# Kernel optimization log

Measured on AMD Instinct MI355X. Metric: run time of the kernel, lower is better.

Reference implementation:

```python
import jax, jax.numpy as jnp
import numpy as np

N_NODES = 100000
N_EDGES = 1250000
N_FEAT = 128
NHID = 64
NUM_GRAPHS = 256


def setup_inputs() -> dict:
    key = jax.random.key(0)
    ks = jax.random.split(key, 12)
    sc = lambda fan_in: 1.414 * (6.0 / fan_in) ** 0.5  # rough xavier-ish scale
    inp = {
        "x": jax.random.normal(ks[0], (N_NODES, N_FEAT), dtype=jnp.float32),
        "edge_attr": jax.random.uniform(ks[1], (N_EDGES, 5), dtype=jnp.float32),
        "W_e1": jax.random.normal(ks[2], (5, NHID), dtype=jnp.float32) * sc(5),
        "b_e1": jnp.zeros((NHID,), jnp.float32),
        "W_e2": jax.random.normal(ks[3], (NHID, NHID), dtype=jnp.float32) * sc(NHID),
        "b_e2": jnp.zeros((NHID,), jnp.float32),
        "W_e3": jax.random.normal(ks[4], (NHID, 1), dtype=jnp.float32) * sc(NHID),
        "b_e3": jnp.zeros((1,), jnp.float32),
        "W_g": jax.random.normal(ks[5], (N_FEAT, NHID), dtype=jnp.float32) * sc(N_FEAT),
        "b_g": jnp.zeros((NHID,), jnp.float32),
        "W_b1": jax.random.normal(ks[6], (NHID, NHID), dtype=jnp.float32) * sc(NHID),
        "b_b1": jnp.zeros((NHID,), jnp.float32),
        "W_b2": jax.random.normal(ks[7], (NHID, 1), dtype=jnp.float32) * sc(NHID),
        "b_b2": jnp.zeros((1,), jnp.float32),
        "edge_index": jax.random.randint(ks[8], (2, N_EDGES), 0, N_NODES, dtype=jnp.int64 if jax.config.jax_enable_x64 else jnp.int32),
        "batch": jnp.sort(jax.random.randint(ks[9], (N_NODES,), 0, NUM_GRAPHS, dtype=jnp.int64 if jax.config.jax_enable_x64 else jnp.int32)),
    }
    return inp


def _forward(x, edge_attr, W_e1, b_e1, W_e2, b_e2, W_e3, b_e3, W_g, b_g,
             W_b1, b_b1, W_b2, b_b2, edge_index, batch):
    N = x.shape[0]
    # edge MLP -> scalar weight per edge, then final ReLU (F.relu in forward)
    h = jax.nn.relu(edge_attr @ W_e1 + b_e1)
    h = jax.nn.relu(h @ W_e2 + b_e2)
    edge_w = jax.nn.relu((h @ W_e3 + b_e3)[:, 0])  # [E]

    row, col = edge_index[0], edge_index[1]
    # add self-loops with weight 1 (PyG GCNConv default)
    loop = jnp.arange(N, dtype=row.dtype)
    row_f = jnp.concatenate([row, loop])
    col_f = jnp.concatenate([col, loop])
    w_f = jnp.concatenate([edge_w, jnp.ones((N,), edge_w.dtype)])

    # symmetric normalization D^{-1/2} A_hat D^{-1/2}
    deg = jax.ops.segment_sum(w_f, col_f, num_segments=N)
    dinv = jnp.where(deg > 0, jax.lax.rsqrt(jnp.where(deg > 0, deg, 1.0)), 0.0)
    norm = dinv[row_f] * w_f * dinv[col_f]  # [E+N]

    xw = x @ W_g  # [N, nhid]
    agg = jax.ops.segment_sum(xw[row_f] * norm[:, None], col_f, num_segments=N)
    node = jax.nn.relu(agg + b_g)  # dropout is identity in eval mode

    pooled = jax.ops.segment_sum(node, batch, num_segments=NUM_GRAPHS)  # [G, nhid]
    z = jax.nn.relu(pooled @ W_b1 + b_b1)
    logits = z @ W_b2 + b_b2  # [G, 1]
    return logits


def reference(x, edge_attr, W_e1, b_e1, W_e2, b_e2, W_e3, b_e3, W_g, b_g,
              W_b1, b_b1, W_b2, b_b2, edge_index, batch):
    return _forward(x, edge_attr, W_e1, b_e1, W_e2, b_e2, W_e3, b_e3, W_g, b_g,
                    W_b1, b_b1, W_b2, b_b2, edge_index, batch)
```

## Files before the change

### kernel.cpp

```cpp
#include <hip/hip_runtime.h>
#include <hip/hip_bf16.h>

#define N_NODES 100000
#define N_EDGES 1250000
#define N_FEAT 128
#define NHID 64
#define NUM_GRAPHS 256
#define NB_SCAN 98

typedef __attribute__((ext_vector_type(8))) short short8;
typedef __attribute__((ext_vector_type(16))) float float16;
typedef __attribute__((ext_vector_type(4))) int int4v;

static __device__ __forceinline__ short f2bf(float x) {
    __hip_bfloat16 b = __float2bfloat16(x);
    return *reinterpret_cast<short*>(&b);
}
static __device__ __forceinline__ float bf2f(short s) {
    __hip_bfloat16 b = *reinterpret_cast<__hip_bfloat16*>(&s);
    return __bfloat162float(b);
}
static __device__ __forceinline__ int pk2(float a, float b) {
    unsigned lo = (unsigned short)f2bf(a);
    unsigned hi = (unsigned short)f2bf(b);
    return (int)(lo | (hi << 16));
}

__global__ void k0_init(int* __restrict__ cnt, float* __restrict__ pooled) {
    int i = blockIdx.x * blockDim.x + threadIdx.x;
    if (i < N_NODES) cnt[i] = 0;
    if (i < NUM_GRAPHS * NHID) pooled[i] = 0.0f;
}

__global__ __launch_bounds__(256) void k1_edge_mlp(
    const float* __restrict__ ea, const float* __restrict__ W1,
    const float* __restrict__ b1, const float* __restrict__ W2,
    const float* __restrict__ b2, const float* __restrict__ W3,
    const float* __restrict__ b3, const int* __restrict__ eidx,
    float* __restrict__ edge_w, int* __restrict__ cnt)
{
    const int lane = threadIdx.x & 63;
    const int l31 = lane & 31;
    const int h = lane >> 5;
    const int wslot = blockIdx.x * 4 + (threadIdx.x >> 6);
    const int S = gridDim.x * 4;
    const float b3v = b3[0];

    short8 a1hi[2], a1lo[2];
    #pragma unroll
    for (int t = 0; t < 2; ++t)
        #pragma unroll
        for (int j = 0; j < 8; ++j) {
            int k = 8 * h + j;
            float v = (k < 5) ? W1[k * NHID + t * 32 + l31] : 0.0f;
            short hi = f2bf(v);
            a1hi[t][j] = hi;
            a1lo[t][j] = f2bf(v - bf2f(hi));
        }

    float b1r[2][16];
    #pragma unroll
    for (int t = 0; t < 2; ++t)
        #pragma unroll
        for (int r = 0; r < 16; ++r)
            b1r[t][r] = b1[t * 32 + (r & 3) + 8 * (r >> 2) + 4 * h];

    short8 afrag[2][4];
    #pragma unroll
    for (int t = 0; t < 2; ++t)
        #pragma unroll
        for (int kk = 0; kk < 4; ++kk)
            #pragma unroll
            for (int j = 0; j < 8; ++j) {
                int k = kk * 16 + h * 8 + j;
                afrag[t][kk][j] = f2bf(W2[k * NHID + t * 32 + l31]);
            }

    float b2r[2][16], w3r[2][16];
    #pragma unroll
    for (int t = 0; t < 2; ++t)
        #pragma unroll
        for (int r = 0; r < 16; ++r) {
            int hid = t * 32 + (r & 3) + 8 * (r >> 2) + 4 * h;
            b2r[t][r] = b2[hid];
            w3r[t][r] = W3[hid];
        }

    const int NCHUNK = (N_EDGES + 31) / 32;

    float pe[5] = {0.f, 0.f, 0.f, 0.f, 0.f};
    if (wslot < NCHUNK && h == 0) {
        int e = wslot * 32 + l31;
        int ec = (e < N_EDGES) ? e : (N_EDGES - 1);
        #pragma unroll
        for (int j = 0; j < 5; ++j) pe[j] = ea[ec * 5 + j];
    }

    for (int chunk = wslot; chunk < NCHUNK; chunk += S) {
        int nchunk = chunk + S;
        float ne[5] = {0.f, 0.f, 0.f, 0.f, 0.f};
        if (nchunk < NCHUNK && h == 0) {
            int e2 = nchunk * 32 + l31;
            int ec2 = (e2 < N_EDGES) ? e2 : (N_EDGES - 1);
            #pragma unroll
            for (int j = 0; j < 5; ++j) ne[j] = ea[ec2 * 5 + j];
        }

        int e = chunk * 32 + l31;
        bool valid = e < N_EDGES;

        short8 behi, belo;
        #pragma unroll
        for (int j = 0; j < 8; ++j) {
            float v = (h == 0 && j < 5) ? pe[j] : 0.0f;
            short hi = f2bf(v);
            behi[j] = hi;
            belo[j] = f2bf(v - bf2f(hi));
        }

        float16 acc1a, acc1b;
        #pragma unroll
        for (int r = 0; r < 16; ++r) { acc1a[r] = b1r[0][r]; acc1b[r] = b1r[1][r]; }
        acc1a = __builtin_amdgcn_mfma_f32_32x32x16_bf16(a1hi[0], behi, acc1a, 0, 0, 0);
        acc1a = __builtin_amdgcn_mfma_f32_32x32x16_bf16(a1hi[0], belo, acc1a, 0, 0, 0);
        acc1a = __builtin_amdgcn_mfma_f32_32x32x16_bf16(a1lo[0], behi, acc1a, 0, 0, 0);
        acc1b = __builtin_amdgcn_mfma_f32_32x32x16_bf16(a1hi[1], behi, acc1b, 0, 0, 0);
        acc1b = __builtin_amdgcn_mfma_f32_32x32x16_bf16(a1hi[1], belo, acc1b, 0, 0, 0);
        acc1b = __builtin_amdgcn_mfma_f32_32x32x16_bf16(a1lo[1], behi, acc1b, 0, 0, 0);

        short8 bf2v[4];
        #pragma unroll
        for (int kk = 0; kk < 4; ++kk) {
            float lv0, lv1, lv2, lv3, hv0, hv1, hv2, hv3;
            if (kk >> 1) {
                int o = 8 * (kk & 1);
                lv0 = fmaxf(acc1b[o + 0], 0.f); lv1 = fmaxf(acc1b[o + 1], 0.f);
                lv2 = fmaxf(acc1b[o + 2], 0.f); lv3 = fmaxf(acc1b[o + 3], 0.f);
                hv0 = fmaxf(acc1b[o + 4], 0.f); hv1 = fmaxf(acc1b[o + 5], 0.f);
                hv2 = fmaxf(acc1b[o + 6], 0.f); hv3 = fmaxf(acc1b[o + 7], 0.f);
            } else {
                int o = 8 * (kk & 1);
                lv0 = fmaxf(acc1a[o + 0], 0.f); lv1 = fmaxf(acc1a[o + 1], 0.f);
                lv2 = fmaxf(acc1a[o + 2], 0.f); lv3 = fmaxf(acc1a[o + 3], 0.f);
                hv0 = fmaxf(acc1a[o + 4], 0.f); hv1 = fmaxf(acc1a[o + 5], 0.f);
                hv2 = fmaxf(acc1a[o + 6], 0.f); hv3 = fmaxf(acc1a[o + 7], 0.f);
            }
            int p_lv0 = pk2(lv0, lv1), p_lv1 = pk2(lv2, lv3);
            int p_hv0 = pk2(hv0, hv1), p_hv1 = pk2(hv2, hv3);
            int send0 = h ? p_lv0 : p_hv0;
            int send1 = h ? p_lv1 : p_hv1;
            int r0 = __shfl_xor(send0, 32, 64);
            int r1 = __shfl_xor(send1, 32, 64);
            int4v fi;
            fi.x = h ? r0 : p_lv0;
            fi.y = h ? r1 : p_lv1;
            fi.z = h ? p_hv0 : r0;
            fi.w = h ? p_hv1 : r1;
            bf2v[kk] = __builtin_bit_cast(short8, fi);
        }

        float16 c0, c1;
        #pragma unroll
        for (int r = 0; r < 16; ++r) { c0[r] = b2r[0][r]; c1[r] = b2r[1][r]; }
        #pragma unroll
        for (int kk = 0; kk < 4; ++kk) {
            c0 = __builtin_amdgcn_mfma_f32_32x32x16_bf16(afrag[0][kk], bf2v[kk], c0, 0, 0, 0);
            c1 = __builtin_amdgcn_mfma_f32_32x32x16_bf16(afrag[1][kk], bf2v[kk], c1, 0, 0, 0);
        }

        float partial = 0.0f;
        #pragma unroll
        for (int r = 0; r < 16; ++r) {
            partial += fmaxf(c0[r], 0.0f) * w3r[0][r];
            partial += fmaxf(c1[r], 0.0f) * w3r[1][r];
        }
        float total = partial + __shfl_xor(partial, 32, 64);
        float w = fmaxf(total + b3v, 0.0f);

        if (h == 0 && valid) {
            edge_w[e] = w;
            if (w > 0.0f) atomicAdd(&cnt[eidx[N_EDGES + e]], 1);
        }

        #pragma unroll
        for (int j = 0; j < 5; ++j) pe[j] = ne[j];
    }
}

__global__ __launch_bounds__(1024) void s1_blocksum(const int* __restrict__ cnt,
                                                    int* __restrict__ bsum) {
    __shared__ int sd[1024];
    int t = threadIdx.x;
    int i = blockIdx.x * 1024 + t;
    sd[t] = (i < N_NODES) ? cnt[i] : 0;
    __syncthreads();
    #pragma unroll
    for (int d = 512; d > 0; d >>= 1) {
        if (t < d) sd[t] += sd[t + d];
        __syncthreads();
    }
    if (t == 0) bsum[blockIdx.x] = sd[0];
}

__global__ __launch_bounds__(128) void s2_scanbase(const int* __restrict__ bsum,
                                                   int* __restrict__ bbase,
                                                   int* __restrict__ off) {
    __shared__ int sd[128];
    int t = threadIdx.x;
    int v = (t < NB_SCAN) ? bsum[t] : 0;
    sd[t] = v;
    __syncthreads();
    #pragma unroll
    for (int d = 1; d < 128; d <<= 1) {
        int u = (t >= d) ? sd[t - d] : 0;
        __syncthreads();
        sd[t] += u;
        __syncthreads();
    }
    if (t < NB_SCAN) bbase[t] = sd[t] - v;
    if (t == 127) off[N_NODES] = sd[127];
}

__global__ __launch_bounds__(1024) void s3_blockscan(const int* __restrict__ cnt,
                                                     const int* __restrict__ bbase,
                                                     int* __restrict__ off,
                                                     int* __restrict__ cur) {
    __shared__ int sd[1024];
    int t = threadIdx.x;
    int i = blockIdx.x * 1024 + t;
    int c = (i < N_NODES) ? cnt[i] : 0;
    sd[t] = c;
    __syncthreads();
    #pragma unroll
    for (int d = 1; d < 1024; d <<= 1) {
        int v = (t >= d) ? sd[t - d] : 0;
        __syncthreads();
        sd[t] += v;
        __syncthreads();
    }
    if (i < N_NODES) {
        int ex = sd[t] - c + bbase[blockIdx.x];
        off[i] = ex;
        cur[i] = ex;
    }
}

__global__ void k_place(const float* __restrict__ edge_w, const int* __restrict__ eidx,
                        int* __restrict__ cur, int2* __restrict__ recs) {
    int e = blockIdx.x * 256 + threadIdx.x;
    if (e >= N_EDGES) return;
    float w = edge_w[e];
    if (w <= 0.0f) return;
    int col = eidx[N_EDGES + e];
    int pos = atomicAdd(&cur[col], 1);
    recs[pos] = make_int2(eidx[e], __float_as_int(w));
}

__global__ void k_deg(const int* __restrict__ off, const int2* __restrict__ recs,
                      float* __restrict__ dinv) {
    int n = blockIdx.x * 256 + threadIdx.x;
    if (n >= N_NODES) return;
    int o0 = off[n], o1 = off[n + 1];
    float s = 1.0f;
    for (int j = o0; j < o1; ++j) s += __int_as_float(recs[j].y);
    dinv[n] = rsqrtf(s);
}

__global__ __launch_bounds__(256) void k3_xw(
    const float* __restrict__ x, const float* __restrict__ Wg,
    const float* __restrict__ dinv, float* __restrict__ xws)
{
    const int lane = threadIdx.x & 63;
    const int l31 = lane & 31;
    const int h = lane >> 5;
    const int wslot = blockIdx.x * 4 + (threadIdx.x >> 6);

    short8 bw[8][2];
    #pragma unroll
    for (int kk = 0; kk < 8; ++kk)
        #pragma unroll
        for (int u = 0; u < 2; ++u)
            #pragma unroll
            for (int j = 0; j < 8; ++j)
                bw[kk][u][j] = f2bf(Wg[(kk * 16 + 8 * h + j) * NHID + u * 32 + l31]);

    const int NC = N_NODES / 32;
    for (int chunk = wslot; chunk < NC; chunk += gridDim.x * 4) {
        int base = chunk * 32;
        const float* xrow = x + (size_t)(base + l31) * N_FEAT + 8 * h;

        float16 acc0, acc1;
        #pragma unroll
        for (int r = 0; r < 16; ++r) { acc0[r] = 0.0f; acc1[r] = 0.0f; }

        #pragma unroll
        for (int kk = 0; kk < 8; ++kk) {
            float4 p = *(const float4*)(xrow + kk * 16);
            float4 q = *(const float4*)(xrow + kk * 16 + 4);
            short8 af;
            af[0] = f2bf(p.x); af[1] = f2bf(p.y); af[2] = f2bf(p.z); af[3] = f2bf(p.w);
            af[4] = f2bf(q.x); af[5] = f2bf(q.y); af[6] = f2bf(q.z); af[7] = f2bf(q.w);
            acc0 = __builtin_amdgcn_mfma_f32_32x32x16_bf16(af, bw[kk][0], acc0, 0, 0, 0);
            acc1 = __builtin_amdgcn_mfma_f32_32x32x16_bf16(af, bw[kk][1], acc1, 0, 0, 0);
        }

        #pragma unroll
        for (int r = 0; r < 16; ++r) {
            int node = base + (r & 3) + 8 * (r >> 2) + 4 * h;
            float dv = dinv[node];
            xws[node * NHID + l31] = acc0[r] * dv;
            xws[node * NHID + 32 + l31] = acc1[r] * dv;
        }
    }
}

__global__ __launch_bounds__(256) void k4_gather_pool(
    const int* __restrict__ off, const int2* __restrict__ recs,
    const float* __restrict__ xws, const float* __restrict__ dinv,
    const float* __restrict__ bg, const int* __restrict__ batch,
    float* __restrict__ pooled)
{
    const int lane = threadIdx.x & 63;
    const int wv = blockIdx.x * 4 + (threadIdx.x >> 6);
    int n0 = wv * 8;
    if (n0 >= N_NODES) return;
    float bgl = bg[lane];
    float pacc = 0.0f;
    int curg = batch[n0];
    #pragma unroll
    for (int nn = 0; nn < 8; ++nn) {
        int n = n0 + nn;
        int g = batch[n];
        if (g != curg) {
            atomicAdd(&pooled[curg * NHID + lane], pacc);
            pacc = 0.0f;
            curg = g;
        }
        int o0 = off[n], o1 = off[n + 1];
        float acc = xws[(size_t)n * NHID + lane];
        if (o0 < o1) {
            int2 r = recs[o0];
            float gth = xws[(size_t)r.x * NHID + lane];
            for (int j = o0; j < o1 - 1; ++j) {
                int2 rn = recs[j + 1];
                float gn = xws[(size_t)rn.x * NHID + lane];
                acc = fmaf(__int_as_float(r.y), gth, acc);
                r = rn; gth = gn;
            }
            acc = fmaf(__int_as_float(r.y), gth, acc);
        }
        pacc += fmaxf(dinv[n] * acc + bgl, 0.0f);
    }
    atomicAdd(&pooled[curg * NHID + lane], pacc);
}

__global__ __launch_bounds__(64) void k6_final(
    const float* __restrict__ pooled, const float* __restrict__ Wb1,
    const float* __restrict__ bb1, const float* __restrict__ Wb2,
    const float* __restrict__ bb2, float* __restrict__ out) {
    __shared__ float p[NHID];
    int lane = threadIdx.x;
    int g = blockIdx.x;
    p[lane] = pooled[g * NHID + lane];
    __syncthreads();
    float z = bb1[lane];
    #pragma unroll
    for (int k = 0; k < NHID; ++k) z += p[k] * Wb1[k * NHID + lane];
    z = fmaxf(z, 0.0f) * Wb2[lane];
    #pragma unroll
    for (int off = 32; off > 0; off >>= 1)
        z += __shfl_down(z, off, 64);
    if (lane == 0) out[g] = z + bb2[0];
}

extern "C" void kernel_launch(void* const* d_in, const int* in_sizes, int n_in,
                              void* d_out, int out_size, void* d_ws, size_t ws_size,
                              hipStream_t stream) {
    const float* x        = (const float*)d_in[0];
    const float* ea       = (const float*)d_in[1];
    const float* W_e1     = (const float*)d_in[2];
    const float* b_e1     = (const float*)d_in[3];
    const float* W_e2     = (const float*)d_in[4];
    const float* b_e2     = (const float*)d_in[5];
    const float* W_e3     = (const float*)d_in[6];
    const float* b_e3     = (const float*)d_in[7];
    const float* W_g      = (const float*)d_in[8];
    const float* b_g      = (const float*)d_in[9];
    const float* W_b1     = (const float*)d_in[10];
    const float* b_b1     = (const float*)d_in[11];
    const float* W_b2     = (const float*)d_in[12];
    const float* b_b2     = (const float*)d_in[13];
    const int*   eidx     = (const int*)d_in[14];
    const int*   batch    = (const int*)d_in[15];
    float* out = (float*)d_out;

    char* wsb = (char*)d_ws;
    float* edge_w = (float*)wsb;
    int*   cnt    = (int*)(wsb + 4 * 1250048);
    int*   off    = (int*)(wsb + 4 * 1350080);
    int*   cur    = (int*)(wsb + 4 * 1450112);
    int*   bsum   = (int*)(wsb + 4 * 1550144);
    int*   bbase  = (int*)(wsb + 4 * 1550272);
    float* dinv   = (float*)(wsb + 4 * 1550400);
    float* pooled = (float*)(wsb + 4 * 1650432);
    int2*  recs   = (int2*)(wsb + 4 * 1666880);
    float* xws    = (float*)(wsb + 4 * 4166880);

    k0_init<<<dim3(391), dim3(256), 0, stream>>>(cnt, pooled);
    k1_edge_mlp<<<dim3(2048), dim3(256), 0, stream>>>(
        ea, W_e1, b_e1, W_e2, b_e2, W_e3, b_e3, eidx, edge_w, cnt);
    s1_blocksum<<<dim3(NB_SCAN), dim3(1024), 0, stream>>>(cnt, bsum);
    s2_scanbase<<<dim3(1), dim3(128), 0, stream>>>(bsum, bbase, off);
    s3_blockscan<<<dim3(NB_SCAN), dim3(1024), 0, stream>>>(cnt, bbase, off, cur);
    k_place<<<dim3((N_EDGES + 255) / 256), dim3(256), 0, stream>>>(edge_w, eidx, cur, recs);
    k_deg<<<dim3((N_NODES + 255) / 256), dim3(256), 0, stream>>>(off, recs, dinv);
    k3_xw<<<dim3(512), dim3(256), 0, stream>>>(x, W_g, dinv, xws);
    k4_gather_pool<<<dim3(3125), dim3(256), 0, stream>>>(off, recs, xws, dinv, b_g, batch, pooled);
    k6_final<<<dim3(NUM_GRAPHS), dim3(64), 0, stream>>>(pooled, W_b1, b_b1, W_b2, b_b2, out);
}
```

Before: 233.3 us.

## Fuse degree computation into edge MLP, fold biases into MFMA, retune gather

The edge MLP now processes two 32-edge chunks per iteration and folds the b1 and b2 biases into the MFMA operands through a constant-one column. It also atomically accumulates float degrees, which removes the separate k_deg pass; dinv is computed inside the block scan. The init kernel is replaced by a memset. The gather kernel handles 4 nodes per wave with a 4-way unrolled edge loop, and the grid sizes change. The cost is extra float atomics per edge, and the bf16 rounding of the b2 bias is a small accuracy risk.

```diff
diff --git a/kernel.cpp b/kernel.cpp
--- a/kernel.cpp
+++ b/kernel.cpp
@@ -26,18 +26,12 @@
     return (int)(lo | (hi << 16));
 }
 
-__global__ void k0_init(int* __restrict__ cnt, float* __restrict__ pooled) {
-    int i = blockIdx.x * blockDim.x + threadIdx.x;
-    if (i < N_NODES) cnt[i] = 0;
-    if (i < NUM_GRAPHS * NHID) pooled[i] = 0.0f;
-}
-
 __global__ __launch_bounds__(256) void k1_edge_mlp(
     const float* __restrict__ ea, const float* __restrict__ W1,
     const float* __restrict__ b1, const float* __restrict__ W2,
     const float* __restrict__ b2, const float* __restrict__ W3,
     const float* __restrict__ b3, const int* __restrict__ eidx,
-    float* __restrict__ edge_w, int* __restrict__ cnt)
+    float* __restrict__ edge_w, int* __restrict__ cnt, float* __restrict__ degf)
 {
     const int lane = threadIdx.x & 63;
     const int l31 = lane & 31;
@@ -52,19 +46,13 @@
         #pragma unroll
         for (int j = 0; j < 8; ++j) {
             int k = 8 * h + j;
-            float v = (k < 5) ? W1[k * NHID + t * 32 + l31] : 0.0f;
+            int m = t * 32 + l31;
+            float v = (k < 5) ? W1[k * NHID + m] : ((k == 5) ? b1[m] : 0.0f);
             short hi = f2bf(v);
             a1hi[t][j] = hi;
             a1lo[t][j] = f2bf(v - bf2f(hi));
         }
 
-    float b1r[2][16];
-    #pragma unroll
-    for (int t = 0; t < 2; ++t)
-        #pragma unroll
-        for (int r = 0; r < 16; ++r)
-            b1r[t][r] = b1[t * 32 + (r & 3) + 8 * (r >> 2) + 4 * h];
-
     short8 afrag[2][4];
     #pragma unroll
     for (int t = 0; t < 2; ++t)
@@ -76,114 +64,139 @@
                 afrag[t][kk][j] = f2bf(W2[k * NHID + t * 32 + l31]);
             }
 
-    float b2r[2][16], w3r[2][16];
+    short8 a2b[2], bone;
     #pragma unroll
     for (int t = 0; t < 2; ++t)
         #pragma unroll
-        for (int r = 0; r < 16; ++r) {
-            int hid = t * 32 + (r & 3) + 8 * (r >> 2) + 4 * h;
-            b2r[t][r] = b2[hid];
-            w3r[t][r] = W3[hid];
-        }
+        for (int j = 0; j < 8; ++j)
+            a2b[t][j] = (h == 0 && j == 0) ? f2bf(b2[t * 32 + l31]) : (short)0;
+    #pragma unroll
+    for (int j = 0; j < 8; ++j)
+        bone[j] = (h == 0 && j == 0) ? f2bf(1.0f) : (short)0;
+
+    float w3r[2][16];
+    #pragma unroll
+    for (int t = 0; t < 2; ++t)
+        #pragma unroll
+        for (int r = 0; r < 16; ++r)
+            w3r[t][r] = W3[t * 32 + (r & 3) + 8 * (r >> 2) + 4 * h];
 
     const int NCHUNK = (N_EDGES + 31) / 32;
-
-    float pe[5] = {0.f, 0.f, 0.f, 0.f, 0.f};
-    if (wslot < NCHUNK && h == 0) {
-        int e = wslot * 32 + l31;
-        int ec = (e < N_EDGES) ? e : (N_EDGES - 1);
-        #pragma unroll
-        for (int j = 0; j < 5; ++j) pe[j] = ea[ec * 5 + j];
-    }
-
-    for (int chunk = wslot; chunk < NCHUNK; chunk += S) {
-        int nchunk = chunk + S;
-        float ne[5] = {0.f, 0.f, 0.f, 0.f, 0.f};
-        if (nchunk < NCHUNK && h == 0) {
-            int e2 = nchunk * 32 + l31;
-            int ec2 = (e2 < N_EDGES) ? e2 : (N_EDGES - 1);
-            #pragma unroll
-            for (int j = 0; j < 5; ++j) ne[j] = ea[ec2 * 5 + j];
-        }
-
-        int e = chunk * 32 + l31;
-        bool valid = e < N_EDGES;
-
-        short8 behi, belo;
-        #pragma unroll
-        for (int j = 0; j < 8; ++j) {
-            float v = (h == 0 && j < 5) ? pe[j] : 0.0f;
-            short hi = f2bf(v);
-            behi[j] = hi;
-            belo[j] = f2bf(v - bf2f(hi));
-        }
-
-        float16 acc1a, acc1b;
-        #pragma unroll
-        for (int r = 0; r < 16; ++r) { acc1a[r] = b1r[0][r]; acc1b[r] = b1r[1][r]; }
-        acc1a = __builtin_amdgcn_mfma_f32_32x32x16_bf16(a1hi[0], behi, acc1a, 0, 0, 0);
-        acc1a = __builtin_amdgcn_mfma_f32_32x32x16_bf16(a1hi[0], belo, acc1a, 0, 0, 0);
-        acc1a = __builtin_amdgcn_mfma_f32_32x32x16_bf16(a1lo[0], behi, acc1a, 0, 0, 0);
-        acc1b = __builtin_amdgcn_mfma_f32_32x32x16_bf16(a1hi[1], behi, acc1b, 0, 0, 0);
-        acc1b = __builtin_amdgcn_mfma_f32_32x32x16_bf16(a1hi[1], belo, acc1b, 0, 0, 0);
-        acc1b = __builtin_amdgcn_mfma_f32_32x32x16_bf16(a1lo[1], behi, acc1b, 0, 0, 0);
-
-        short8 bf2v[4];
-        #pragma unroll
-        for (int kk = 0; kk < 4; ++kk) {
-            float lv0, lv1, lv2, lv3, hv0, hv1, hv2, hv3;
-            if (kk >> 1) {
+    const int PAIRS = (NCHUNK + 1) / 2;
+
+    for (int p = wslot; p < PAIRS; p += S) {
+        int ch[2] = {2 * p, 2 * p + 1};
+
+        short8 behi[2], belo[2];
+        bool cvq[2];
+        #pragma unroll
+        for (int q = 0; q < 2; ++q) {
+            int e = ch[q] * 32 + l31;
+            cvq[q] = (ch[q] < NCHUNK) && (e < N_EDGES);
+            int ec = (e < N_EDGES) ? e : (N_EDGES - 1);
+            #pragma unroll
+            for (int j = 0; j < 8; ++j) {
+                float v = 0.0f;
+                if (h == 0) {
+                    if (j < 5) v = ea[ec * 5 + j];
+                    else if (j == 5) v = 1.0f;
+                }
+                short hi = f2bf(v);
+                behi[q][j] = hi;
+                belo[q][j] = (h == 0 && j < 5) ? f2bf(v - bf2f(hi)) : (short)0;
+            }
+        }
+
+        float16 A1[2][2];
+        #pragma unroll
+        for (int q = 0; q < 2; ++q)
+            #pragma unroll
+            for (int t = 0; t < 2; ++t)
+                #pragma unroll
+                for (int r = 0; r < 16; ++r) A1[q][t][r] = 0.0f;
+        #pragma unroll
+        for (int t = 0; t < 2; ++t)
+            #pragma unroll
+            for (int q = 0; q < 2; ++q) {
+                A1[q][t] = __builtin_amdgcn_mfma_f32_32x32x16_bf16(a1hi[t], behi[q], A1[q][t], 0, 0, 0);
+                A1[q][t] = __builtin_amdgcn_mfma_f32_32x32x16_bf16(a1hi[t], belo[q], A1[q][t], 0, 0, 0);
+                A1[q][t] = __builtin_amdgcn_mfma_f32_32x32x16_bf16(a1lo[t], behi[q], A1[q][t], 0, 0, 0);
+            }
+
+        short8 bf2v[2][4];
+        #pragma unroll
+        for (int q = 0; q < 2; ++q) {
+            #pragma unroll
+            for (int kk = 0; kk < 4; ++kk) {
+                float lv0, lv1, lv2, lv3, hv0, hv1, hv2, hv3;
                 int o = 8 * (kk & 1);
-                lv0 = fmaxf(acc1b[o + 0], 0.f); lv1 = fmaxf(acc1b[o + 1], 0.f);
-                lv2 = fmaxf(acc1b[o + 2], 0.f); lv3 = fmaxf(acc1b[o + 3], 0.f);
-                hv0 = fmaxf(acc1b[o + 4], 0.f); hv1 = fmaxf(acc1b[o + 5], 0.f);
-                hv2 = fmaxf(acc1b[o + 6], 0.f); hv3 = fmaxf(acc1b[o + 7], 0.f);
-            } else {
-                int o = 8 * (kk & 1);
-                lv0 = fmaxf(acc1a[o + 0], 0.f); lv1 = fmaxf(acc1a[o + 1], 0.f);
-                lv2 = fmaxf(acc1a[o + 2], 0.f); lv3 = fmaxf(acc1a[o + 3], 0.f);
-                hv0 = fmaxf(acc1a[o + 4], 0.f); hv1 = fmaxf(acc1a[o + 5], 0.f);
-                hv2 = fmaxf(acc1a[o + 6], 0.f); hv3 = fmaxf(acc1a[o + 7], 0.f);
-            }
-            int p_lv0 = pk2(lv0, lv1), p_lv1 = pk2(lv2, lv3);
-            int p_hv0 = pk2(hv0, hv1), p_hv1 = pk2(hv2, hv3);
-            int send0 = h ? p_lv0 : p_hv0;
-            int send1 = h ? p_lv1 : p_hv1;
-            int r0 = __shfl_xor(send0, 32, 64);
-            int r1 = __shfl_xor(send1, 32, 64);
-            int4v fi;
-            fi.x = h ? r0 : p_lv0;
-            fi.y = h ? r1 : p_lv1;
-            fi.z = h ? p_hv0 : r0;
-            fi.w = h ? p_hv1 : r1;
-            bf2v[kk] = __builtin_bit_cast(short8, fi);
-        }
-
-        float16 c0, c1;
-        #pragma unroll
-        for (int r = 0; r < 16; ++r) { c0[r] = b2r[0][r]; c1[r] = b2r[1][r]; }
-        #pragma unroll
-        for (int kk = 0; kk < 4; ++kk) {
-            c0 = __builtin_amdgcn_mfma_f32_32x32x16_bf16(afrag[0][kk], bf2v[kk], c0, 0, 0, 0);
-            c1 = __builtin_amdgcn_mfma_f32_32x32x16_bf16(afrag[1][kk], bf2v[kk], c1, 0, 0, 0);
-        }
-
-        float partial = 0.0f;
-        #pragma unroll
-        for (int r = 0; r < 16; ++r) {
-            partial += fmaxf(c0[r], 0.0f) * w3r[0][r];
-            partial += fmaxf(c1[r], 0.0f) * w3r[1][r];
-        }
-        float total = partial + __shfl_xor(partial, 32, 64);
-        float w = fmaxf(total + b3v, 0.0f);
-
-        if (h == 0 && valid) {
-            edge_w[e] = w;
-            if (w > 0.0f) atomicAdd(&cnt[eidx[N_EDGES + e]], 1);
-        }
-
-        #pragma unroll
-        for (int j = 0; j < 5; ++j) pe[j] = ne[j];
+                if (kk >> 1) {
+                    lv0 = fmaxf(A1[q][1][o + 0], 0.f); lv1 = fmaxf(A1[q][1][o + 1], 0.f);
+                    lv2 = fmaxf(A1[q][1][o + 2], 0.f); lv3 = fmaxf(A1[q][1][o + 3], 0.f);
+                    hv0 = fmaxf(A1[q][1][o + 4], 0.f); hv1 = fmaxf(A1[q][1][o + 5], 0.f);
+                    hv2 = fmaxf(A1[q][1][o + 6], 0.f); hv3 = fmaxf(A1[q][1][o + 7], 0.f);
+                } else {
+                    lv0 = fmaxf(A1[q][0][o + 0], 0.f); lv1 = fmaxf(A1[q][0][o + 1], 0.f);
+                    lv2 = fmaxf(A1[q][0][o + 2], 0.f); lv3 = fmaxf(A1[q][0][o + 3], 0.f);
+                    hv0 = fmaxf(A1[q][0][o + 4], 0.f); hv1 = fmaxf(A1[q][0][o + 5], 0.f);
+                    hv2 = fmaxf(A1[q][0][o + 6], 0.f); hv3 = fmaxf(A1[q][0][o + 7], 0.f);
+                }
+                int p_lv0 = pk2(lv0, lv1), p_lv1 = pk2(lv2, lv3);
+                int p_hv0 = pk2(hv0, hv1), p_hv1 = pk2(hv2, hv3);
+                int send0 = h ? p_lv0 : p_hv0;
+                int send1 = h ? p_lv1 : p_hv1;
+                int r0 = __shfl_xor(send0, 32, 64);
+                int r1 = __shfl_xor(send1, 32, 64);
+                int4v fi;
+                fi.x = h ? r0 : p_lv0;
+                fi.y = h ? r1 : p_lv1;
+                fi.z = h ? p_hv0 : r0;
+                fi.w = h ? p_hv1 : r1;
+                bf2v[q][kk] = __builtin_bit_cast(short8, fi);
+            }
+        }
+
+        float16 C[2][2];
+        #pragma unroll
+        for (int q = 0; q < 2; ++q)
+            #pragma unroll
+            for (int t = 0; t < 2; ++t)
+                #pragma unroll
+                for (int r = 0; r < 16; ++r) C[q][t][r] = 0.0f;
+        #pragma unroll
+        for (int kk = 0; kk < 4; ++kk)
+            #pragma unroll
+            for (int q = 0; q < 2; ++q) {
+                C[q][0] = __builtin_amdgcn_mfma_f32_32x32x16_bf16(afrag[0][kk], bf2v[q][kk], C[q][0], 0, 0, 0);
+                C[q][1] = __builtin_amdgcn_mfma_f32_32x32x16_bf16(afrag[1][kk], bf2v[q][kk], C[q][1], 0, 0, 0);
+            }
+        #pragma unroll
+        for (int q = 0; q < 2; ++q) {
+            C[q][0] = __builtin_amdgcn_mfma_f32_32x32x16_bf16(a2b[0], bone, C[q][0], 0, 0, 0);
+            C[q][1] = __builtin_amdgcn_mfma_f32_32x32x16_bf16(a2b[1], bone, C[q][1], 0, 0, 0);
+        }
+
+        #pragma unroll
+        for (int q = 0; q < 2; ++q) {
+            float partial = 0.0f;
+            #pragma unroll
+            for (int r = 0; r < 16; ++r) {
+                partial += fmaxf(C[q][0][r], 0.0f) * w3r[0][r];
+                partial += fmaxf(C[q][1][r], 0.0f) * w3r[1][r];
+            }
+            float total = partial + __shfl_xor(partial, 32, 64);
+            float w = fmaxf(total + b3v, 0.0f);
+
+            if (h == 0 && cvq[q]) {
+                int e = ch[q] * 32 + l31;
+                edge_w[e] = w;
+                if (w > 0.0f) {
+                    int col = eidx[N_EDGES + e];
+                    atomicAdd(&cnt[col], 1);
+                    atomicAdd(&degf[col], w);
+                }
+            }
+        }
     }
 }
 
@@ -224,7 +237,9 @@
 __global__ __launch_bounds__(1024) void s3_blockscan(const int* __restrict__ cnt,
                                                      const int* __restrict__ bbase,
                                                      int* __restrict__ off,
-                                                     int* __restrict__ cur) {
+                                                     int* __restrict__ cur,
+                                                     const float* __restrict__ degf,
+                                                     float* __restrict__ dinv) {
     __shared__ int sd[1024];
     int t = threadIdx.x;
     int i = blockIdx.x * 1024 + t;
@@ -242,6 +257,7 @@
         int ex = sd[t] - c + bbase[blockIdx.x];
         off[i] = ex;
         cur[i] = ex;
+        dinv[i] = rsqrtf(1.0f + degf[i]);
     }
 }
 
@@ -256,16 +272,6 @@
     recs[pos] = make_int2(eidx[e], __float_as_int(w));
 }
 
-__global__ void k_deg(const int* __restrict__ off, const int2* __restrict__ recs,
-                      float* __restrict__ dinv) {
-    int n = blockIdx.x * 256 + threadIdx.x;
-    if (n >= N_NODES) return;
-    int o0 = off[n], o1 = off[n + 1];
-    float s = 1.0f;
-    for (int j = o0; j < o1; ++j) s += __int_as_float(recs[j].y);
-    dinv[n] = rsqrtf(s);
-}
-
 __global__ __launch_bounds__(256) void k3_xw(
     const float* __restrict__ x, const float* __restrict__ Wg,
     const float* __restrict__ dinv, float* __restrict__ xws)
@@ -322,14 +328,13 @@
 {
     const int lane = threadIdx.x & 63;
     const int wv = blockIdx.x * 4 + (threadIdx.x >> 6);
-    int n0 = wv * 8;
+    int n0 = wv * 4;
     if (n0 >= N_NODES) return;
+    int n1 = min(n0 + 4, N_NODES);
     float bgl = bg[lane];
     float pacc = 0.0f;
     int curg = batch[n0];
-    #pragma unroll
-    for (int nn = 0; nn < 8; ++nn) {
-        int n = n0 + nn;
+    for (int n = n0; n < n1; ++n) {
         int g = batch[n];
         if (g != curg) {
             atomicAdd(&pooled[curg * NHID + lane], pacc);
@@ -338,16 +343,21 @@
         }
         int o0 = off[n], o1 = off[n + 1];
         float acc = xws[(size_t)n * NHID + lane];
-        if (o0 < o1) {
-            int2 r = recs[o0];
-            float gth = xws[(size_t)r.x * NHID + lane];
-            for (int j = o0; j < o1 - 1; ++j) {
-                int2 rn = recs[j + 1];
-                float gn = xws[(size_t)rn.x * NHID + lane];
-                acc = fmaf(__int_as_float(r.y), gth, acc);
-                r = rn; gth = gn;
-            }
-            acc = fmaf(__int_as_float(r.y), gth, acc);
+        int j = o0;
+        for (; j + 4 <= o1; j += 4) {
+            int2 r0 = recs[j], r1 = recs[j + 1], r2 = recs[j + 2], r3 = recs[j + 3];
+            float g0 = xws[(size_t)r0.x * NHID + lane];
+            float g1 = xws[(size_t)r1.x * NHID + lane];
+            float g2 = xws[(size_t)r2.x * NHID + lane];
+            float g3 = xws[(size_t)r3.x * NHID + lane];
+            acc = fmaf(__int_as_float(r0.y), g0, acc);
+            acc = fmaf(__int_as_float(r1.y), g1, acc);
+            acc = fmaf(__int_as_float(r2.y), g2, acc);
+            acc = fmaf(__int_as_float(r3.y), g3, acc);
+        }
+        for (; j < o1; ++j) {
+            int2 r = recs[j];
+            acc = fmaf(__int_as_float(r.y), xws[(size_t)r.x * NHID + lane], acc);
         }
         pacc += fmaxf(dinv[n] * acc + bgl, 0.0f);
     }
@@ -395,26 +405,27 @@
     float* out = (float*)d_out;
 
     char* wsb = (char*)d_ws;
-    float* edge_w = (float*)wsb;
-    int*   cnt    = (int*)(wsb + 4 * 1250048);
-    int*   off    = (int*)(wsb + 4 * 1350080);
-    int*   cur    = (int*)(wsb + 4 * 1450112);
-    int*   bsum   = (int*)(wsb + 4 * 1550144);
-    int*   bbase  = (int*)(wsb + 4 * 1550272);
-    float* dinv   = (float*)(wsb + 4 * 1550400);
-    float* pooled = (float*)(wsb + 4 * 1650432);
-    int2*  recs   = (int2*)(wsb + 4 * 1666880);
-    float* xws    = (float*)(wsb + 4 * 4166880);
-
-    k0_init<<<dim3(391), dim3(256), 0, stream>>>(cnt, pooled);
-    k1_edge_mlp<<<dim3(2048), dim3(256), 0, stream>>>(
-        ea, W_e1, b_e1, W_e2, b_e2, W_e3, b_e3, eidx, edge_w, cnt);
+    int*   cnt    = (int*)wsb;
+    float* degf   = (float*)(wsb + 4 * 100000);
+    float* pooled = (float*)(wsb + 4 * 200000);
+    float* edge_w = (float*)(wsb + 4 * 216448);
+    int*   off    = (int*)(wsb + 4 * 1466448);
+    int*   cur    = (int*)(wsb + 4 * 1566456);
+    int*   bsum   = (int*)(wsb + 4 * 1666456);
+    int*   bbase  = (int*)(wsb + 4 * 1666560);
+    int2*  recs   = (int2*)(wsb + 4 * 1666688);
+    float* dinv   = (float*)(wsb + 4 * 4166688);
+    float* xws    = (float*)(wsb + 4 * 4266688);
+
+    hipMemsetAsync(wsb, 0, 4 * 216384, stream);
+
+    k1_edge_mlp<<<dim3(1024), dim3(256), 0, stream>>>(
+        ea, W_e1, b_e1, W_e2, b_e2, W_e3, b_e3, eidx, edge_w, cnt, degf);
     s1_blocksum<<<dim3(NB_SCAN), dim3(1024), 0, stream>>>(cnt, bsum);
     s2_scanbase<<<dim3(1), dim3(128), 0, stream>>>(bsum, bbase, off);
-    s3_blockscan<<<dim3(NB_SCAN), dim3(1024), 0, stream>>>(cnt, bbase, off, cur);
+    s3_blockscan<<<dim3(NB_SCAN), dim3(1024), 0, stream>>>(cnt, bbase, off, cur, degf, dinv);
     k_place<<<dim3((N_EDGES + 255) / 256), dim3(256), 0, stream>>>(edge_w, eidx, cur, recs);
-    k_deg<<<dim3((N_NODES + 255) / 256), dim3(256), 0, stream>>>(off, recs, dinv);
     k3_xw<<<dim3(512), dim3(256), 0, stream>>>(x, W_g, dinv, xws);
-    k4_gather_pool<<<dim3(3125), dim3(256), 0, stream>>>(off, recs, xws, dinv, b_g, batch, pooled);
+    k4_gather_pool<<<dim3(6250), dim3(256), 0, stream>>>(off, recs, xws, dinv, b_g, batch, pooled);
     k6_final<<<dim3(NUM_GRAPHS), dim3(64), 0, stream>>>(pooled, W_b1, b_b1, W_b2, b_b2, out);
 }
```

Result: faster. 223.5 us (-4.2%).
